# Kernel optimization log

Hardware: AMD Instinct MI355X
Metric: run time of the kernel (lower is better)

The kernel has to match this reference:

```python
import jax, jax.numpy as jnp
import numpy as np

E, B, D, H, Z = 8, 16384, 512, 512, 64   # experts, batch, input_dim, hidden, latent
NHID = 2                                 # num_mlp_layers - 1 hidden-to-hidden layers


def setup_inputs() -> dict:
    key = jax.random.key(0)
    ks = jax.random.split(key, 12)

    def w(k, shape, fan_in):
        return (jax.random.normal(k, shape, jnp.float32) / np.sqrt(fan_in)).astype(jnp.float32)

    return {
        "x": jax.random.normal(ks[0], (B, D), jnp.float32),
        "eps": jax.random.normal(ks[1], (B, Z), jnp.float32),
        # stacked per-expert parameters (leading axis E)
        "enc_in_w": w(ks[2], (E, D, H), D), "enc_in_b": jnp.zeros((E, H), jnp.float32),
        "enc_hid_w": w(ks[3], (E, NHID, H, H), H), "enc_hid_b": jnp.zeros((E, NHID, H), jnp.float32),
        "mu_w": w(ks[4], (E, H, Z), H), "mu_b": jnp.zeros((E, Z), jnp.float32),
        "lv_w": w(ks[5], (E, H, Z), H), "lv_b": jnp.zeros((E, Z), jnp.float32),
        "dec_in_w": w(ks[6], (E, Z, H), Z), "dec_in_b": jnp.zeros((E, H), jnp.float32),
        "dec_hid_w": w(ks[7], (E, NHID, H, H), H), "dec_hid_b": jnp.zeros((E, NHID, H), jnp.float32),
        "dec_out_w": w(ks[8], (E, H, D), H), "dec_out_b": jnp.zeros((E, D), jnp.float32),
    }


def _moe_forward(x, eps, enc_in_w, enc_in_b, enc_hid_w, enc_hid_b,
                 mu_w, mu_b, lv_w, lv_b,
                 dec_in_w, dec_in_b, dec_hid_w, dec_hid_b, dec_out_w, dec_out_b):
    # ---- every expert tries the problem (dense, all experts over full batch) ----
    h = jax.nn.relu(jnp.einsum('bd,edh->ebh', x, enc_in_w) + enc_in_b[:, None, :])
    for i in range(NHID):
        h = jax.nn.relu(jnp.einsum('ebh,ehk->ebk', h, enc_hid_w[:, i]) + enc_hid_b[:, i, None, :])
    mu = jnp.einsum('ebh,ehz->ebz', h, mu_w) + mu_b[:, None, :]          # [E,B,Z]
    logvar = jnp.einsum('ebh,ehz->ebz', h, lv_w) + lv_b[:, None, :]       # [E,B,Z]
    z = mu + jnp.exp(0.5 * logvar) * eps[None, :, :]                      # reparameterize
    g = jax.nn.relu(jnp.einsum('ebz,ezh->ebh', z, dec_in_w) + dec_in_b[:, None, :])
    for i in range(NHID):
        g = jax.nn.relu(jnp.einsum('ebh,ehk->ebk', g, dec_hid_w[:, i]) + dec_hid_b[:, i, None, :])
    xhat = jnp.einsum('ebh,ehd->ebd', g, dec_out_w) + dec_out_b[:, None, :]  # [E,B,D]

    # ---- per-sample recon loss, pick best expert (torch.min over experts) ----
    recon = jnp.mean((xhat - x[None, :, :]) ** 2, axis=-1)                # [E,B]
    expert_idx = jnp.argmin(recon, axis=0)                                # [B]

    # ---- sparse_others: single fused gather instead of python loop ----
    bi = jnp.arange(x.shape[0])
    return mu[expert_idx, bi], logvar[expert_idx, bi], xhat[expert_idx, bi]


def reference(x, eps, enc_in_w, enc_in_b, enc_hid_w, enc_hid_b,
              mu_w, mu_b, lv_w, lv_b,
              dec_in_w, dec_in_b, dec_hid_w, dec_hid_b, dec_out_w, dec_out_b):
    return _moe_forward(x, eps, enc_in_w, enc_in_b, enc_hid_w, enc_hid_b,
                        mu_w, mu_b, lv_w, lv_b,
                        dec_in_w, dec_in_b, dec_hid_w, dec_hid_b, dec_out_w, dec_out_b)
```

## Files before the change

kernel.cpp:

```cpp
#include <hip/hip_runtime.h>
#include <cstdint>

#define Eexp 8
#define Bb   16384
#define Dd   512
#define Hh   512
#define Zz   64

typedef _Float16 f16x8 __attribute__((ext_vector_type(8)));
typedef _Float16 f16x4 __attribute__((ext_vector_type(4)));
typedef float    f32x4 __attribute__((ext_vector_type(4)));

#define OFF_ENCIN  0
#define OFF_HID0   524288
#define OFF_HID1   1048576
#define OFF_HEADS  1572864
#define OFF_DECIN  1703936
#define OFF_DHID0  1769472
#define OFF_DHID1  2293760
#define OFF_DECOUT 2818048
#define PEREXP     3342336
#define WT_TOTAL   (8 * (size_t)PEREXP)

#define GLL16(g, l) __builtin_amdgcn_global_load_lds( \
    (const __attribute__((address_space(1))) void*)(g), \
    (__attribute__((address_space(3))) void*)(l), 16, 0, 0)

template<bool TR>
__global__ __launch_bounds__(256)
void fmsplit(const float* __restrict__ src, _Float16* __restrict__ dst,
             int KTOT, int inner, long sStride, long dStride)
{
    __shared__ float t[64][65];
    const int e  = blockIdx.z;
    const int o0 = blockIdx.x * 64;
    const int k0 = blockIdx.y * 64;
    const float* S = src + (size_t)e * sStride;
    _Float16*    D = dst + (size_t)e * dStride;
    const int tid = threadIdx.x;
    const int rr = tid >> 4, c4 = (tid & 15) * 4;
    #pragma unroll
    for (int p = 0; p < 4; ++p) {
        const int r = rr + p * 16;
        const float4 v = *reinterpret_cast<const float4*>(
            S + (size_t)(TR ? (k0 + r) : (o0 + r)) * inner + (TR ? o0 : k0) + c4);
        t[r][c4 + 0] = v.x; t[r][c4 + 1] = v.y;
        t[r][c4 + 2] = v.z; t[r][c4 + 3] = v.w;
    }
    __syncthreads();
    const int lane = tid & 63, wid = tid >> 6;
    const int KB = KTOT >> 5;
    #pragma unroll
    for (int p = 0; p < 2; ++p) {
        const int g  = wid * 2 + p;
        const int ot = g >> 1, kb = g & 1;
        const int rI = ot * 16 + (lane & 15);
        const int kI = kb * 32 + (lane >> 4) * 8;
        f16x8 hv, lv;
        #pragma unroll
        for (int j = 0; j < 8; ++j) {
            const float v = TR ? t[kI + j][rI] : t[rI][kI + j];
            const _Float16 h = (_Float16)v;
            hv[j] = h; lv[j] = (_Float16)(v - (float)h);
        }
        const size_t base = ((size_t)((o0 >> 4) + ot) * KB + (k0 >> 5) + kb) * 1024;
        *reinterpret_cast<f16x8*>(D + base + lane * 8)       = hv;
        *reinterpret_cast<f16x8*>(D + base + 512 + lane * 8) = lv;
    }
}

__global__ __launch_bounds__(256)
void zfm_kernel(const float* __restrict__ mu, const float* __restrict__ lv,
                const float* __restrict__ eps, _Float16* __restrict__ zfm)
{
    __shared__ float t[64][65];
    const int r0 = blockIdx.x * 64;
    const int tid = threadIdx.x, rr = tid >> 4, c4 = (tid & 15) * 4;
    #pragma unroll
    for (int p = 0; p < 4; ++p) {
        const int r = rr + p * 16;
        const size_t o = (size_t)(r0 + r) * 64 + c4;
        const float4 m = *reinterpret_cast<const float4*>(mu + o);
        const float4 l = *reinterpret_cast<const float4*>(lv + o);
        const float4 e = *reinterpret_cast<const float4*>(eps + o);
        t[r][c4 + 0] = m.x + expf(0.5f * l.x) * e.x;
        t[r][c4 + 1] = m.y + expf(0.5f * l.y) * e.y;
        t[r][c4 + 2] = m.z + expf(0.5f * l.z) * e.z;
        t[r][c4 + 3] = m.w + expf(0.5f * l.w) * e.w;
    }
    __syncthreads();
    const int lane = tid & 63, wid = tid >> 6;
    #pragma unroll
    for (int p = 0; p < 2; ++p) {
        const int g  = wid * 2 + p;
        const int ot = g >> 1, kb = g & 1;
        const int rI = ot * 16 + (lane & 15);
        const int kI = kb * 32 + (lane >> 4) * 8;
        f16x8 hv, lvv;
        #pragma unroll
        for (int j = 0; j < 8; ++j) {
            const float v = t[rI][kI + j];
            const _Float16 h = (_Float16)v;
            hv[j] = h; lvv[j] = (_Float16)(v - (float)h);
        }
        const size_t base = ((size_t)((r0 >> 4) + ot) * 2 + kb) * 1024;
        *reinterpret_cast<f16x8*>(zfm + base + lane * 8)       = hv;
        *reinterpret_cast<f16x8*>(zfm + base + 512 + lane * 8) = lvv;
    }
}

template<int KA, int MODE>
__global__ __launch_bounds__(512, 2)
void gemm8(const _Float16* __restrict__ Afm, const _Float16* __restrict__ Wfm,
           const float* __restrict__ bias0, const float* __restrict__ bias1,
           float* __restrict__ Cf, float* __restrict__ Cf1,
           _Float16* __restrict__ Cfm, const float* __restrict__ Xin,
           float* __restrict__ rec8)
{
    constexpr bool BIG = (MODE != 2);
    constexpr int BM  = BIG ? 256 : 64;
    constexpr int KB  = KA / 32;
    constexpr int NT  = KB;
    constexpr int ACH = BIG ? 32 : 8;
    constexpr int NCH = BIG ? 48 : 24;
    constexpr int CPW = NCH / 8;
    constexpr int NF  = BIG ? 4 : 1;
    __shared__ __align__(16) _Float16 lds[2 * NCH * 512];

    const int bid = blockIdx.x;
    const int logical = (bid & 7) * 32 + (bid >> 3);
    const int bx = BIG ? (logical & 63) : logical;
    const int by = BIG ? (logical >> 6) : 0;

    const int lane = threadIdx.x & 63, wid = threadIdx.x >> 6;
    const int wr = BIG ? (wid >> 1) : 0;
    const int wc = BIG ? (wid & 1) : wid;
    const int row0 = bx * BM;
    const int col0 = by * 128;

    const _Float16* src[CPW];
    #pragma unroll
    for (int p = 0; p < CPW; ++p) {
        const int q = wid * CPW + p;
        if (q < ACH) {
            const int T = q >> 1, pl = q & 1;
            src[p] = Afm + (size_t)((row0 >> 4) + T) * KB * 1024 + pl * 512 + lane * 8;
        } else {
            const int T = (q - ACH) >> 1, pl = q & 1;
            src[p] = Wfm + (size_t)((col0 >> 4) + T) * KB * 1024 + pl * 512 + lane * 8;
        }
    }

    f32x4 acc[4][NF];
    #pragma unroll
    for (int i = 0; i < 4; ++i)
        #pragma unroll
        for (int j = 0; j < NF; ++j) acc[i][j] = {0.f, 0.f, 0.f, 0.f};

#define STAGE_H(buf, h)                                                      \
    { _Pragma("unroll")                                                      \
      for (int p = (h) * 3; p < ((h) ? CPW : 3); ++p) {                      \
          GLL16(src[p], lds + (buf) * (NCH * 512) + (wid * CPW + p) * 512);  \
          src[p] += 1024;                                                    \
      } }

    STAGE_H(0, 0) STAGE_H(0, 1)

    for (int t = 0; t < NT; ++t) {
        const int b = t & 1;
        const _Float16* B0 = lds + b * (NCH * 512);

        if (t + 1 < NT) STAGE_H(b ^ 1, 0)
        if (t + 1 < NT) { asm volatile("s_waitcnt vmcnt(3)" ::: "memory"); }
        else            { asm volatile("s_waitcnt vmcnt(0)" ::: "memory"); }
        __builtin_amdgcn_s_barrier();
        asm volatile("" ::: "memory");

        f16x8 ah[4], al[4], wh[NF], wl[NF];
        #pragma unroll
        for (int mf = 0; mf < 4; ++mf) {
            const int q = (wr * 4 + mf) << 1;
            ah[mf] = *reinterpret_cast<const f16x8*>(B0 + q * 512 + lane * 8);
            al[mf] = *reinterpret_cast<const f16x8*>(B0 + q * 512 + 512 + lane * 8);
        }
        constexpr int NF0 = BIG ? 2 : 1;
        #pragma unroll
        for (int nf = 0; nf < NF0; ++nf) {
            const int q = ACH + ((wc * NF + nf) << 1);
            wh[nf] = *reinterpret_cast<const f16x8*>(B0 + q * 512 + lane * 8);
            wl[nf] = *reinterpret_cast<const f16x8*>(B0 + q * 512 + 512 + lane * 8);
        }
        __builtin_amdgcn_s_setprio(1);
        #pragma unroll
        for (int mf = 0; mf < 4; ++mf)
            #pragma unroll
            for (int nf = 0; nf < NF0; ++nf) {
                acc[mf][nf] = __builtin_amdgcn_mfma_f32_16x16x32_f16(
                    ah[mf], wh[nf], acc[mf][nf], 0, 0, 0);
                acc[mf][nf] = __builtin_amdgcn_mfma_f32_16x16x32_f16(
                    ah[mf], wl[nf], acc[mf][nf], 0, 0, 0);
                acc[mf][nf] = __builtin_amdgcn_mfma_f32_16x16x32_f16(
                    al[mf], wh[nf], acc[mf][nf], 0, 0, 0);
            }
        __builtin_amdgcn_s_setprio(0);
        asm volatile("" ::: "memory");
        __builtin_amdgcn_s_barrier();
        asm volatile("" ::: "memory");

        if constexpr (BIG) {
            if (t + 1 < NT) STAGE_H(b ^ 1, 1)
            #pragma unroll
            for (int nf = 2; nf < 4; ++nf) {
                const int q = ACH + ((wc * NF + nf) << 1);
                wh[nf] = *reinterpret_cast<const f16x8*>(B0 + q * 512 + lane * 8);
                wl[nf] = *reinterpret_cast<const f16x8*>(B0 + q * 512 + 512 + lane * 8);
            }
            __builtin_amdgcn_s_setprio(1);
            #pragma unroll
            for (int mf = 0; mf < 4; ++mf)
                #pragma unroll
                for (int nf = 2; nf < 4; ++nf) {
                    acc[mf][nf] = __builtin_amdgcn_mfma_f32_16x16x32_f16(
                        ah[mf], wh[nf], acc[mf][nf], 0, 0, 0);
                    acc[mf][nf] = __builtin_amdgcn_mfma_f32_16x16x32_f16(
                        ah[mf], wl[nf], acc[mf][nf], 0, 0, 0);
                    acc[mf][nf] = __builtin_amdgcn_mfma_f32_16x16x32_f16(
                        al[mf], wh[nf], acc[mf][nf], 0, 0, 0);
                }
            __builtin_amdgcn_s_setprio(0);
            asm volatile("" ::: "memory");
            __builtin_amdgcn_s_barrier();
            asm volatile("" ::: "memory");
        }
    }
#undef STAGE_H

    if constexpr (MODE == 0) {
        uint32_t* sb = reinterpret_cast<uint32_t*>(&lds[0]);
        #pragma unroll
        for (int ph = 0; ph < 2; ++ph) {
            if (wc == ph) {
                #pragma unroll
                for (int nf = 0; nf < NF; ++nf) {
                    const int c_l = nf * 16 + (lane & 15);
                    const float bv = bias0[col0 + wc * 64 + c_l];
                    #pragma unroll
                    for (int mf = 0; mf < 4; ++mf)
                        #pragma unroll
                        for (int j = 0; j < 4; ++j) {
                            const int r_l = wr * 64 + mf * 16 + (lane >> 4) * 4 + j;
                            const float v = fmaxf(acc[mf][nf][j] + bv, 0.f);
                            const _Float16 h = (_Float16)v;
                            const _Float16 lo = (_Float16)(v - (float)h);
                            const uint32_t pk =
                                (uint32_t)__builtin_bit_cast(uint16_t, h) |
                                ((uint32_t)__builtin_bit_cast(uint16_t, lo) << 16);
                            sb[r_l * 64 + (((c_l >> 2) ^ (r_l & 15)) << 2) + (c_l & 3)] = pk;
                        }
                }
            }
            __syncthreads();
            if (wc == ph) {
                #pragma unroll
                for (int T_l = 0; T_l < 4; ++T_l)
                    #pragma unroll
                    for (int kb_l = 0; kb_l < 2; ++kb_l) {
                        const int r_l = wr * 64 + T_l * 16 + (lane & 15);
                        const int cb  = kb_l * 32 + (lane >> 4) * 8;
                        uint32_t u[8];
                        #pragma unroll
                        for (int jb = 0; jb < 2; ++jb) {
                            const int chunk = ((cb >> 2) + jb) ^ (r_l & 15);
                            const uint32_t* pp = &sb[r_l * 64 + chunk * 4];
                            u[jb*4+0] = pp[0]; u[jb*4+1] = pp[1];
                            u[jb*4+2] = pp[2]; u[jb*4+3] = pp[3];
                        }
                        f16x8 hv, lvv;
                        #pragma unroll
                        for (int j = 0; j < 8; ++j) {
                            hv[j]  = __builtin_bit_cast(_Float16, (uint16_t)(u[j] & 0xffff));
                            lvv[j] = __builtin_bit_cast(_Float16, (uint16_t)(u[j] >> 16));
                        }
                        const size_t base =
                            ((size_t)((row0 >> 4) + wr * 4 + T_l) * 16 +
                             (col0 >> 5) + wc * 2 + kb_l) * 1024;
                        *reinterpret_cast<f16x8*>(Cfm + base + lane * 8)       = hv;
                        *reinterpret_cast<f16x8*>(Cfm + base + 512 + lane * 8) = lvv;
                    }
            }
            __syncthreads();
        }
    } else if constexpr (MODE == 1) {
        float rsum[4][4];
        #pragma unroll
        for (int mf = 0; mf < 4; ++mf)
            #pragma unroll
            for (int j = 0; j < 4; ++j) rsum[mf][j] = 0.f;
        #pragma unroll
        for (int nf = 0; nf < NF; ++nf) {
            const int col = col0 + wc * 64 + nf * 16 + (lane & 15);
            const float bv = bias0[col];
            #pragma unroll
            for (int mf = 0; mf < 4; ++mf)
                #pragma unroll
                for (int j = 0; j < 4; ++j) {
                    const int row = row0 + wr * 64 + mf * 16 + (lane >> 4) * 4 + j;
                    const float v = acc[mf][nf][j] + bv;
                    Cf[(size_t)row * 512 + col] = v;
                    const float d = v - Xin[(size_t)row * 512 + col];
                    rsum[mf][j] += d * d;
                }
        }
        #pragma unroll
        for (int mf = 0; mf < 4; ++mf)
            #pragma unroll
            for (int j = 0; j < 4; ++j) {
                float s = rsum[mf][j];
                s += __shfl_xor(s, 1); s += __shfl_xor(s, 2);
                s += __shfl_xor(s, 4); s += __shfl_xor(s, 8);
                if ((lane & 15) == 0) {
                    const int row = row0 + wr * 64 + mf * 16 + (lane >> 4) * 4 + j;
                    rec8[(size_t)(by * 2 + wc) * Bb + row] = s;
                }
            }
    } else {
        const int c_h = wc * 16 + (lane & 15);
        const float bv = (c_h < 64) ? bias0[c_h] : bias1[c_h - 64];
        float* CP = (c_h < 64) ? Cf : Cf1;
        const int c = c_h & 63;
        #pragma unroll
        for (int mf = 0; mf < 4; ++mf)
            #pragma unroll
            for (int j = 0; j < 4; ++j) {
                const int row = row0 + mf * 16 + (lane >> 4) * 4 + j;
                CP[(size_t)row * 64 + c] = acc[mf][0][j] + bv;
            }
    }
}

__global__ __launch_bounds__(256)
void select_kernel(const float* __restrict__ rec8, float* __restrict__ best,
                   const float* __restrict__ mu_e, const float* __restrict__ lv_e,
                   const float* __restrict__ xhat,
                   float* __restrict__ out_mu, float* __restrict__ out_lv,
                   float* __restrict__ out_xh, int isFirst)
{
    const int wave = threadIdx.x >> 6;
    const int lane = threadIdx.x & 63;
    const int row  = blockIdx.x * 4 + wave;
    float r = 0.f;
    #pragma unroll
    for (int p = 0; p < 8; ++p) r += rec8[(size_t)p * Bb + row];
    r *= (1.0f / 512.0f);
    const bool cond = isFirst || (r < best[row]);
    if (cond) {
        if (lane == 0) best[row] = r;
        out_mu[(size_t)row * Zz + lane] = mu_e[(size_t)row * Zz + lane];
        out_lv[(size_t)row * Zz + lane] = lv_e[(size_t)row * Zz + lane];
        const float4* src = reinterpret_cast<const float4*>(&xhat[(size_t)row * Dd]);
        float4*       dst = reinterpret_cast<float4*>(&out_xh[(size_t)row * Dd]);
        dst[lane]      = src[lane];
        dst[lane + 64] = src[lane + 64];
    }
}

extern "C" void kernel_launch(void* const* d_in, const int* in_sizes, int n_in,
                              void* d_out, int out_size, void* d_ws, size_t ws_size,
                              hipStream_t stream)
{
    const float* x         = (const float*)d_in[0];
    const float* eps       = (const float*)d_in[1];
    const float* enc_in_w  = (const float*)d_in[2];
    const float* enc_in_b  = (const float*)d_in[3];
    const float* enc_hid_w = (const float*)d_in[4];
    const float* enc_hid_b = (const float*)d_in[5];
    const float* mu_w      = (const float*)d_in[6];
    const float* mu_b      = (const float*)d_in[7];
    const float* lv_w      = (const float*)d_in[8];
    const float* lv_b      = (const float*)d_in[9];
    const float* dec_in_w  = (const float*)d_in[10];
    const float* dec_in_b  = (const float*)d_in[11];
    const float* dec_hid_w = (const float*)d_in[12];
    const float* dec_hid_b = (const float*)d_in[13];
    const float* dec_out_w = (const float*)d_in[14];
    const float* dec_out_b = (const float*)d_in[15];

    const size_t FM = (size_t)Bb * 512 * 2;
    const size_t BZ = (size_t)Bb * 64;

    _Float16* wt  = (_Float16*)d_ws;
    _Float16* xfm = wt + WT_TOTAL;
    _Float16* afm = xfm + FM;
    _Float16* bfm = afm + FM;
    _Float16* zfm = bfm + FM;
    float* fbase  = (float*)(zfm + (size_t)Bb * 64 * 2);
    float* xhat   = fbase;
    float* mu_e   = xhat + (size_t)Bb * 512;
    float* lv_e   = mu_e + BZ;
    float* rec8   = lv_e + BZ;
    float* best   = rec8 + (size_t)8 * Bb;

    float* out_mu = (float*)d_out;
    float* out_lv = out_mu + (size_t)Bb * Zz;
    float* out_xh = out_lv + (size_t)Bb * Zz;

    const dim3 blk(256);

    fmsplit<true ><<<dim3(8, 8, 8), blk, 0, stream>>>(enc_in_w,           wt + OFF_ENCIN,  512, 512, 262144, PEREXP);
    fmsplit<true ><<<dim3(8, 8, 8), blk, 0, stream>>>(enc_hid_w,          wt + OFF_HID0,   512, 512, 524288, PEREXP);
    fmsplit<true ><<<dim3(8, 8, 8), blk, 0, stream>>>(enc_hid_w + 262144, wt + OFF_HID1,   512, 512, 524288, PEREXP);
    fmsplit<true ><<<dim3(1, 8, 8), blk, 0, stream>>>(mu_w,               wt + OFF_HEADS,  512,  64,  32768, PEREXP);
    fmsplit<true ><<<dim3(1, 8, 8), blk, 0, stream>>>(lv_w,        wt + OFF_HEADS + 65536, 512,  64,  32768, PEREXP);
    fmsplit<true ><<<dim3(8, 1, 8), blk, 0, stream>>>(dec_in_w,           wt + OFF_DECIN,   64, 512,  32768, PEREXP);
    fmsplit<true ><<<dim3(8, 8, 8), blk, 0, stream>>>(dec_hid_w,          wt + OFF_DHID0,  512, 512, 524288, PEREXP);
    fmsplit<true ><<<dim3(8, 8, 8), blk, 0, stream>>>(dec_hid_w + 262144, wt + OFF_DHID1,  512, 512, 524288, PEREXP);
    fmsplit<true ><<<dim3(8, 8, 8), blk, 0, stream>>>(dec_out_w,          wt + OFF_DECOUT, 512, 512, 262144, PEREXP);
    fmsplit<false><<<dim3(256, 8, 1), blk, 0, stream>>>(x,                xfm,             512, 512, 0, 0);

    const dim3 g256(256), gblk(512), gRow(Bb / 4), gZ(Bb / 64);

    for (int e = 0; e < Eexp; ++e) {
        const _Float16* we = wt + (size_t)e * PEREXP;
        gemm8<512, 0><<<g256, gblk, 0, stream>>>(
            xfm, we + OFF_ENCIN, enc_in_b + (size_t)e * Hh, nullptr,
            nullptr, nullptr, afm, nullptr, nullptr);
        gemm8<512, 0><<<g256, gblk, 0, stream>>>(
            afm, we + OFF_HID0, enc_hid_b + ((size_t)e * 2 + 0) * Hh, nullptr,
            nullptr, nullptr, bfm, nullptr, nullptr);
        gemm8<512, 0><<<g256, gblk, 0, stream>>>(
            bfm, we + OFF_HID1, enc_hid_b + ((size_t)e * 2 + 1) * Hh, nullptr,
            nullptr, nullptr, afm, nullptr, nullptr);
        gemm8<512, 2><<<g256, gblk, 0, stream>>>(
            afm, we + OFF_HEADS, mu_b + (size_t)e * Zz, lv_b + (size_t)e * Zz,
            mu_e, lv_e, nullptr, nullptr, nullptr);
        zfm_kernel<<<gZ, blk, 0, stream>>>(mu_e, lv_e, eps, zfm);
        gemm8< 64, 0><<<g256, gblk, 0, stream>>>(
            zfm, we + OFF_DECIN, dec_in_b + (size_t)e * Hh, nullptr,
            nullptr, nullptr, bfm, nullptr, nullptr);
        gemm8<512, 0><<<g256, gblk, 0, stream>>>(
            bfm, we + OFF_DHID0, dec_hid_b + ((size_t)e * 2 + 0) * Hh, nullptr,
            nullptr, nullptr, afm, nullptr, nullptr);
        gemm8<512, 0><<<g256, gblk, 0, stream>>>(
            afm, we + OFF_DHID1, dec_hid_b + ((size_t)e * 2 + 1) * Hh, nullptr,
            nullptr, nullptr, bfm, nullptr, nullptr);
        gemm8<512, 1><<<g256, gblk, 0, stream>>>(
            bfm, we + OFF_DECOUT, dec_out_b + (size_t)e * Dd, nullptr,
            xhat, nullptr, nullptr, x, rec8);
        select_kernel<<<gRow, blk, 0, stream>>>(
            rec8, best, mu_e, lv_e, xhat, out_mu, out_lv, out_xh, e == 0 ? 1 : 0);
    }
}
```

Measured before the change: 2.000 ms.

## Restructure GEMM: 128x128 tiles, 256 threads, weights loaded straight into registers

The fused split-fp16 GEMM moves from 512-thread blocks with 256x128 tiles to 256-thread blocks with 128x128 tiles, doubling the grid to 512 blocks. Weight fragments are now read from global memory directly into double-buffered registers, and only the activation tiles go through a two-slot LDS ring. This shrinks LDS per block and removes the weight LDS round trip and one barrier phase per K-step, aiming for better occupancy and latency hiding. The cost is more register pressure, and each weight fragment is re-read from global/L2 by every wave that uses it instead of being shared through LDS.

```diff
diff --git a/kernel.cpp b/kernel.cpp
--- a/kernel.cpp
+++ b/kernel.cpp
@@ -8,7 +8,6 @@
 #define Zz   64
 
 typedef _Float16 f16x8 __attribute__((ext_vector_type(8)));
-typedef _Float16 f16x4 __attribute__((ext_vector_type(4)));
 typedef float    f32x4 __attribute__((ext_vector_type(4)));
 
 #define OFF_ENCIN  0
@@ -110,140 +109,124 @@
 }
 
 template<int KA, int MODE>
-__global__ __launch_bounds__(512, 2)
-void gemm8(const _Float16* __restrict__ Afm, const _Float16* __restrict__ Wfm,
+__global__ __launch_bounds__(256, 2)
+void gemm9(const _Float16* __restrict__ Afm, const _Float16* __restrict__ Wfm,
            const float* __restrict__ bias0, const float* __restrict__ bias1,
            float* __restrict__ Cf, float* __restrict__ Cf1,
            _Float16* __restrict__ Cfm, const float* __restrict__ Xin,
            float* __restrict__ rec8)
 {
     constexpr bool BIG = (MODE != 2);
-    constexpr int BM  = BIG ? 256 : 64;
+    constexpr int MF  = BIG ? 4 : 2;
     constexpr int KB  = KA / 32;
     constexpr int NT  = KB;
-    constexpr int ACH = BIG ? 32 : 8;
-    constexpr int NCH = BIG ? 48 : 24;
-    constexpr int CPW = NCH / 8;
-    constexpr int NF  = BIG ? 4 : 1;
-    __shared__ __align__(16) _Float16 lds[2 * NCH * 512];
+    constexpr int ACH = BIG ? 16 : 8;
+    constexpr int GPW = ACH / 4;
+    constexpr int VC  = GPW + 8;
+    __shared__ __align__(16) uint8_t smem[BIG ? 32768 : 16384];
+    _Float16* ring = reinterpret_cast<_Float16*>(smem);
 
     const int bid = blockIdx.x;
-    const int logical = (bid & 7) * 32 + (bid >> 3);
-    const int bx = BIG ? (logical & 63) : logical;
-    const int by = BIG ? (logical >> 6) : 0;
+    int bx, by;
+    if (BIG) { const int idx = bid >> 3; bx = (bid & 7) * 16 + (idx >> 2); by = idx & 3; }
+    else     { bx = (bid & 7) * 32 + (bid >> 3); by = 0; }
 
     const int lane = threadIdx.x & 63, wid = threadIdx.x >> 6;
-    const int wr = BIG ? (wid >> 1) : 0;
-    const int wc = BIG ? (wid & 1) : wid;
-    const int row0 = bx * BM;
+    const int wr = wid >> 1, wc = wid & 1;
+    const int row0 = bx * (BIG ? 128 : 64);
     const int col0 = by * 128;
-
-    const _Float16* src[CPW];
-    #pragma unroll
-    for (int p = 0; p < CPW; ++p) {
-        const int q = wid * CPW + p;
-        if (q < ACH) {
-            const int T = q >> 1, pl = q & 1;
-            src[p] = Afm + (size_t)((row0 >> 4) + T) * KB * 1024 + pl * 512 + lane * 8;
-        } else {
-            const int T = (q - ACH) >> 1, pl = q & 1;
-            src[p] = Wfm + (size_t)((col0 >> 4) + T) * KB * 1024 + pl * 512 + lane * 8;
-        }
-    }
-
-    f32x4 acc[4][NF];
-    #pragma unroll
-    for (int i = 0; i < 4; ++i)
-        #pragma unroll
-        for (int j = 0; j < NF; ++j) acc[i][j] = {0.f, 0.f, 0.f, 0.f};
-
-#define STAGE_H(buf, h)                                                      \
+    const int ct0  = (BIG ? (col0 >> 4) : 0) + wc * 4;
+
+    const _Float16* aSrc[GPW];
+    #pragma unroll
+    for (int p = 0; p < GPW; ++p) {
+        const int q = wid * GPW + p;
+        aSrc[p] = Afm + (size_t)((row0 >> 4) + (q >> 1)) * KB * 1024
+                      + (q & 1) * 512 + lane * 8;
+    }
+    const _Float16* wSrc[8];
+    #pragma unroll
+    for (int i = 0; i < 8; ++i)
+        wSrc[i] = Wfm + (size_t)(ct0 + (i >> 1)) * KB * 1024
+                      + (i & 1) * 512 + lane * 8;
+
+    f32x4 acc[MF][4];
+    #pragma unroll
+    for (int i = 0; i < MF; ++i)
+        #pragma unroll
+        for (int j = 0; j < 4; ++j) acc[i][j] = {0.f, 0.f, 0.f, 0.f};
+
+    f16x8 wA[4][2], wB[4][2];
+
+#define STAGE_A(buf)                                                         \
     { _Pragma("unroll")                                                      \
-      for (int p = (h) * 3; p < ((h) ? CPW : 3); ++p) {                      \
-          GLL16(src[p], lds + (buf) * (NCH * 512) + (wid * CPW + p) * 512);  \
-          src[p] += 1024;                                                    \
+      for (int p = 0; p < GPW; ++p) {                                        \
+          GLL16(aSrc[p], ring + (buf) * (ACH * 512) + (wid * GPW + p) * 512);\
+          aSrc[p] += 1024;                                                   \
       } }
 
-    STAGE_H(0, 0) STAGE_H(0, 1)
-
-    for (int t = 0; t < NT; ++t) {
-        const int b = t & 1;
-        const _Float16* B0 = lds + b * (NCH * 512);
-
-        if (t + 1 < NT) STAGE_H(b ^ 1, 0)
-        if (t + 1 < NT) { asm volatile("s_waitcnt vmcnt(3)" ::: "memory"); }
-        else            { asm volatile("s_waitcnt vmcnt(0)" ::: "memory"); }
-        __builtin_amdgcn_s_barrier();
-        asm volatile("" ::: "memory");
-
-        f16x8 ah[4], al[4], wh[NF], wl[NF];
-        #pragma unroll
-        for (int mf = 0; mf < 4; ++mf) {
-            const int q = (wr * 4 + mf) << 1;
-            ah[mf] = *reinterpret_cast<const f16x8*>(B0 + q * 512 + lane * 8);
-            al[mf] = *reinterpret_cast<const f16x8*>(B0 + q * 512 + 512 + lane * 8);
-        }
-        constexpr int NF0 = BIG ? 2 : 1;
-        #pragma unroll
-        for (int nf = 0; nf < NF0; ++nf) {
-            const int q = ACH + ((wc * NF + nf) << 1);
-            wh[nf] = *reinterpret_cast<const f16x8*>(B0 + q * 512 + lane * 8);
-            wl[nf] = *reinterpret_cast<const f16x8*>(B0 + q * 512 + 512 + lane * 8);
-        }
-        __builtin_amdgcn_s_setprio(1);
-        #pragma unroll
-        for (int mf = 0; mf < 4; ++mf)
-            #pragma unroll
-            for (int nf = 0; nf < NF0; ++nf) {
-                acc[mf][nf] = __builtin_amdgcn_mfma_f32_16x16x32_f16(
-                    ah[mf], wh[nf], acc[mf][nf], 0, 0, 0);
-                acc[mf][nf] = __builtin_amdgcn_mfma_f32_16x16x32_f16(
-                    ah[mf], wl[nf], acc[mf][nf], 0, 0, 0);
-                acc[mf][nf] = __builtin_amdgcn_mfma_f32_16x16x32_f16(
-                    al[mf], wh[nf], acc[mf][nf], 0, 0, 0);
-            }
-        __builtin_amdgcn_s_setprio(0);
-        asm volatile("" ::: "memory");
-        __builtin_amdgcn_s_barrier();
-        asm volatile("" ::: "memory");
-
-        if constexpr (BIG) {
-            if (t + 1 < NT) STAGE_H(b ^ 1, 1)
-            #pragma unroll
-            for (int nf = 2; nf < 4; ++nf) {
-                const int q = ACH + ((wc * NF + nf) << 1);
-                wh[nf] = *reinterpret_cast<const f16x8*>(B0 + q * 512 + lane * 8);
-                wl[nf] = *reinterpret_cast<const f16x8*>(B0 + q * 512 + 512 + lane * 8);
-            }
-            __builtin_amdgcn_s_setprio(1);
-            #pragma unroll
-            for (int mf = 0; mf < 4; ++mf)
-                #pragma unroll
-                for (int nf = 2; nf < 4; ++nf) {
-                    acc[mf][nf] = __builtin_amdgcn_mfma_f32_16x16x32_f16(
-                        ah[mf], wh[nf], acc[mf][nf], 0, 0, 0);
-                    acc[mf][nf] = __builtin_amdgcn_mfma_f32_16x16x32_f16(
-                        ah[mf], wl[nf], acc[mf][nf], 0, 0, 0);
-                    acc[mf][nf] = __builtin_amdgcn_mfma_f32_16x16x32_f16(
-                        al[mf], wh[nf], acc[mf][nf], 0, 0, 0);
-                }
-            __builtin_amdgcn_s_setprio(0);
-            asm volatile("" ::: "memory");
-            __builtin_amdgcn_s_barrier();
-            asm volatile("" ::: "memory");
-        }
-    }
-#undef STAGE_H
+#define LOAD_W(dst)                                                          \
+    { _Pragma("unroll")                                                      \
+      for (int i = 0; i < 8; ++i) {                                          \
+          dst[i >> 1][i & 1] = *reinterpret_cast<const f16x8*>(wSrc[i]);     \
+          wSrc[i] += 1024;                                                   \
+      } }
+
+    STAGE_A(0) LOAD_W(wA)
+    STAGE_A(1) LOAD_W(wB)
+
+#define ITER(t, buf, wset)                                                   \
+    {                                                                        \
+        if ((t) + 1 < NT) { asm volatile("s_waitcnt vmcnt(%0)" :: "i"(VC) : "memory"); } \
+        else              { asm volatile("s_waitcnt vmcnt(0)" ::: "memory"); } \
+        __builtin_amdgcn_s_barrier();                                        \
+        asm volatile("" ::: "memory");                                       \
+        f16x8 ah[MF], al[MF];                                                \
+        _Pragma("unroll")                                                    \
+        for (int mf = 0; mf < MF; ++mf) {                                    \
+            const int q = (wr * MF + mf) * 2;                                \
+            ah[mf] = *reinterpret_cast<const f16x8*>(                        \
+                ring + (buf) * (ACH * 512) + q * 512 + lane * 8);            \
+            al[mf] = *reinterpret_cast<const f16x8*>(                        \
+                ring + (buf) * (ACH * 512) + q * 512 + 512 + lane * 8);      \
+        }                                                                    \
+        __builtin_amdgcn_s_setprio(1);                                       \
+        _Pragma("unroll")                                                    \
+        for (int mf = 0; mf < MF; ++mf)                                      \
+            _Pragma("unroll")                                                \
+            for (int nf = 0; nf < 4; ++nf) {                                 \
+                acc[mf][nf] = __builtin_amdgcn_mfma_f32_16x16x32_f16(        \
+                    ah[mf], wset[nf][0], acc[mf][nf], 0, 0, 0);              \
+                acc[mf][nf] = __builtin_amdgcn_mfma_f32_16x16x32_f16(        \
+                    ah[mf], wset[nf][1], acc[mf][nf], 0, 0, 0);              \
+                acc[mf][nf] = __builtin_amdgcn_mfma_f32_16x16x32_f16(        \
+                    al[mf], wset[nf][0], acc[mf][nf], 0, 0, 0);              \
+            }                                                                \
+        __builtin_amdgcn_s_setprio(0);                                       \
+        if ((t) + 2 < NT) LOAD_W(wset)                                       \
+        asm volatile("" ::: "memory");                                       \
+        __builtin_amdgcn_s_barrier();                                        \
+        asm volatile("" ::: "memory");                                       \
+        if ((t) + 2 < NT) STAGE_A(buf)                                       \
+    }
+
+    for (int t = 0; t < NT; t += 2) {
+        ITER(t,     0, wA)
+        ITER(t + 1, 1, wB)
+    }
+#undef ITER
+#undef LOAD_W
+#undef STAGE_A
 
     if constexpr (MODE == 0) {
-        uint32_t* sb = reinterpret_cast<uint32_t*>(&lds[0]);
+        uint32_t* sb = reinterpret_cast<uint32_t*>(smem);
         #pragma unroll
         for (int ph = 0; ph < 2; ++ph) {
             if (wc == ph) {
                 #pragma unroll
-                for (int nf = 0; nf < NF; ++nf) {
+                for (int nf = 0; nf < 4; ++nf) {
                     const int c_l = nf * 16 + (lane & 15);
-                    const float bv = bias0[col0 + wc * 64 + c_l];
+                    const float bv = bias0[col0 + ph * 64 + c_l];
                     #pragma unroll
                     for (int mf = 0; mf < 4; ++mf)
                         #pragma unroll
@@ -260,33 +243,33 @@
                 }
             }
             __syncthreads();
-            if (wc == ph) {
+            {
                 #pragma unroll
-                for (int T_l = 0; T_l < 4; ++T_l)
+                for (int i = 0; i < 4; ++i) {
+                    const int q = wid * 4 + i;
+                    const int T_l = q >> 1, kb_l = q & 1;
+                    const int r_l = T_l * 16 + (lane & 15);
+                    const int cb  = kb_l * 32 + (lane >> 4) * 8;
+                    uint32_t u[8];
                     #pragma unroll
-                    for (int kb_l = 0; kb_l < 2; ++kb_l) {
-                        const int r_l = wr * 64 + T_l * 16 + (lane & 15);
-                        const int cb  = kb_l * 32 + (lane >> 4) * 8;
-                        uint32_t u[8];
-                        #pragma unroll
-                        for (int jb = 0; jb < 2; ++jb) {
-                            const int chunk = ((cb >> 2) + jb) ^ (r_l & 15);
-                            const uint32_t* pp = &sb[r_l * 64 + chunk * 4];
-                            u[jb*4+0] = pp[0]; u[jb*4+1] = pp[1];
-                            u[jb*4+2] = pp[2]; u[jb*4+3] = pp[3];
-                        }
-                        f16x8 hv, lvv;
-                        #pragma unroll
-                        for (int j = 0; j < 8; ++j) {
-                            hv[j]  = __builtin_bit_cast(_Float16, (uint16_t)(u[j] & 0xffff));
-                            lvv[j] = __builtin_bit_cast(_Float16, (uint16_t)(u[j] >> 16));
-                        }
-                        const size_t base =
-                            ((size_t)((row0 >> 4) + wr * 4 + T_l) * 16 +
-                             (col0 >> 5) + wc * 2 + kb_l) * 1024;
-                        *reinterpret_cast<f16x8*>(Cfm + base + lane * 8)       = hv;
-                        *reinterpret_cast<f16x8*>(Cfm + base + 512 + lane * 8) = lvv;
+                    for (int jb = 0; jb < 2; ++jb) {
+                        const int chunk = ((cb >> 2) + jb) ^ (r_l & 15);
+                        const uint32_t* pp = &sb[r_l * 64 + chunk * 4];
+                        u[jb*4+0] = pp[0]; u[jb*4+1] = pp[1];
+                        u[jb*4+2] = pp[2]; u[jb*4+3] = pp[3];
                     }
+                    f16x8 hv, lvv;
+                    #pragma unroll
+                    for (int j = 0; j < 8; ++j) {
+                        hv[j]  = __builtin_bit_cast(_Float16, (uint16_t)(u[j] & 0xffff));
+                        lvv[j] = __builtin_bit_cast(_Float16, (uint16_t)(u[j] >> 16));
+                    }
+                    const size_t base =
+                        ((size_t)((row0 >> 4) + T_l) * 16 +
+                         ((col0 + ph * 64) >> 5) + kb_l) * 1024;
+                    *reinterpret_cast<f16x8*>(Cfm + base + lane * 8)       = hv;
+                    *reinterpret_cast<f16x8*>(Cfm + base + 512 + lane * 8) = lvv;
+                }
             }
             __syncthreads();
         }
@@ -297,7 +280,7 @@
             #pragma unroll
             for (int j = 0; j < 4; ++j) rsum[mf][j] = 0.f;
         #pragma unroll
-        for (int nf = 0; nf < NF; ++nf) {
+        for (int nf = 0; nf < 4; ++nf) {
             const int col = col0 + wc * 64 + nf * 16 + (lane & 15);
             const float bv = bias0[col];
             #pragma unroll
@@ -324,17 +307,20 @@
                 }
             }
     } else {
-        const int c_h = wc * 16 + (lane & 15);
-        const float bv = (c_h < 64) ? bias0[c_h] : bias1[c_h - 64];
-        float* CP = (c_h < 64) ? Cf : Cf1;
-        const int c = c_h & 63;
-        #pragma unroll
-        for (int mf = 0; mf < 4; ++mf)
+        #pragma unroll
+        for (int nf = 0; nf < 4; ++nf) {
+            const int c_h = wc * 64 + nf * 16 + (lane & 15);
+            const float bv = (c_h < 64) ? bias0[c_h] : bias1[c_h - 64];
+            float* CP = (c_h < 64) ? Cf : Cf1;
+            const int c = c_h & 63;
             #pragma unroll
-            for (int j = 0; j < 4; ++j) {
-                const int row = row0 + mf * 16 + (lane >> 4) * 4 + j;
-                CP[(size_t)row * 64 + c] = acc[mf][0][j] + bv;
-            }
+            for (int mf = 0; mf < MF; ++mf)
+                #pragma unroll
+                for (int j = 0; j < 4; ++j) {
+                    const int row = row0 + wr * 32 + mf * 16 + (lane >> 4) * 4 + j;
+                    CP[(size_t)row * 64 + c] = acc[mf][nf][j] + bv;
+                }
+        }
     }
 }
 
@@ -417,33 +403,33 @@
     fmsplit<true ><<<dim3(8, 8, 8), blk, 0, stream>>>(dec_out_w,          wt + OFF_DECOUT, 512, 512, 262144, PEREXP);
     fmsplit<false><<<dim3(256, 8, 1), blk, 0, stream>>>(x,                xfm,             512, 512, 0, 0);
 
-    const dim3 g256(256), gblk(512), gRow(Bb / 4), gZ(Bb / 64);
+    const dim3 g512(512), g256(256), gRow(Bb / 4), gZ(Bb / 64);
 
     for (int e = 0; e < Eexp; ++e) {
         const _Float16* we = wt + (size_t)e * PEREXP;
-        gemm8<512, 0><<<g256, gblk, 0, stream>>>(
+        gemm9<512, 0><<<g512, blk, 0, stream>>>(
             xfm, we + OFF_ENCIN, enc_in_b + (size_t)e * Hh, nullptr,
             nullptr, nullptr, afm, nullptr, nullptr);
-        gemm8<512, 0><<<g256, gblk, 0, stream>>>(
+        gemm9<512, 0><<<g512, blk, 0, stream>>>(
             afm, we + OFF_HID0, enc_hid_b + ((size_t)e * 2 + 0) * Hh, nullptr,
             nullptr, nullptr, bfm, nullptr, nullptr);
-        gemm8<512, 0><<<g256, gblk, 0, stream>>>(
+        gemm9<512, 0><<<g512, blk, 0, stream>>>(
             bfm, we + OFF_HID1, enc_hid_b + ((size_t)e * 2 + 1) * Hh, nullptr,
             nullptr, nullptr, afm, nullptr, nullptr);
-        gemm8<512, 2><<<g256, gblk, 0, stream>>>(
+        gemm9<512, 2><<<g256, blk, 0, stream>>>(
             afm, we + OFF_HEADS, mu_b + (size_t)e * Zz, lv_b + (size_t)e * Zz,
             mu_e, lv_e, nullptr, nullptr, nullptr);
         zfm_kernel<<<gZ, blk, 0, stream>>>(mu_e, lv_e, eps, zfm);
-        gemm8< 64, 0><<<g256, gblk, 0, stream>>>(
+        gemm9< 64, 0><<<g512, blk, 0, stream>>>(
             zfm, we + OFF_DECIN, dec_in_b + (size_t)e * Hh, nullptr,
             nullptr, nullptr, bfm, nullptr, nullptr);
-        gemm8<512, 0><<<g256, gblk, 0, stream>>>(
+        gemm9<512, 0><<<g512, blk, 0, stream>>>(
             bfm, we + OFF_DHID0, dec_hid_b + ((size_t)e * 2 + 0) * Hh, nullptr,
             nullptr, nullptr, afm, nullptr, nullptr);
-        gemm8<512, 0><<<g256, gblk, 0, stream>>>(
+        gemm9<512, 0><<<g512, blk, 0, stream>>>(
             afm, we + OFF_DHID1, dec_hid_b + ((size_t)e * 2 + 1) * Hh, nullptr,
             nullptr, nullptr, bfm, nullptr, nullptr);
-        gemm8<512, 1><<<g256, gblk, 0, stream>>>(
+        gemm9<512, 1><<<g512, blk, 0, stream>>>(
             bfm, we + OFF_DECOUT, dec_out_b + (size_t)e * Dd, nullptr,
             xhat, nullptr, nullptr, x, rec8);
         select_kernel<<<gRow, blk, 0, stream>>>(
```

Measured after the change: 1.814 ms. 1.1x faster.
